# Optimization experiments

Hardware: AMD Instinct MI355X
Metric: run time of the kernel (lower is better)

Reference implementation:

```python
import jax, jax.numpy as jnp
import numpy as np

N = 50000      # nodes
E = 1600000    # edges (before self loops)
B = 512        # graphs
D = 128        # gcn dim (constant across the 3 GAT layers)
H = 1024       # hidden_dim
O = 128        # output_dim
NEG_SLOPE = 0.2


def setup_inputs() -> dict:
    key = jax.random.key(0)
    ks = jax.random.split(key, 24)
    inp = {
        "x": jax.random.normal(ks[0], (N, D), jnp.float32),
        "edge_index": jax.random.randint(ks[1], (2, E), 0, N, dtype=jnp.int64),
        "edge_weight": jax.random.uniform(ks[2], (E,), jnp.float32),
        "batch": jnp.sort(jax.random.randint(ks[3], (N,), 0, B, dtype=jnp.int64)),
    }
    s = 1.0 / np.sqrt(D)
    for i in range(3):
        k = 4 + 4 * i
        inp[f"W{i+1}"] = jax.random.normal(ks[k], (D, D), jnp.float32) * s
        inp[f"as{i+1}"] = jax.random.normal(ks[k + 1], (D,), jnp.float32) * s
        inp[f"ad{i+1}"] = jax.random.normal(ks[k + 2], (D,), jnp.float32) * s
        inp[f"b{i+1}"] = jnp.zeros((D,), jnp.float32)
    inp["Wf1"] = jax.random.normal(ks[16], (D, H), jnp.float32) * s
    inp["bf1"] = jnp.zeros((H,), jnp.float32)
    inp["Wf2"] = jax.random.normal(ks[17], (H, O), jnp.float32) * (1.0 / np.sqrt(H))
    inp["bf2"] = jnp.zeros((O,), jnp.float32)
    return inp


def gat_conv(x, src, dst, W, a_src, a_dst, b):
    """PyG GATConv, heads=1: gather -> leakyrelu -> segment softmax -> scatter-add."""
    h = x @ W                                   # [N, D]
    e = jax.nn.leaky_relu(jnp.take(h @ a_src, src) + jnp.take(h @ a_dst, dst), NEG_SLOPE)  # [E']
    m = jax.ops.segment_max(e, dst, num_segments=N)
    ex = jnp.exp(e - m[dst])
    denom = jax.ops.segment_sum(ex, dst, num_segments=N)
    alpha = ex / denom[dst]                      # segment softmax over incoming edges
    out = jax.ops.segment_sum(alpha[:, None] * h[src], dst, num_segments=N)
    return out + b


def reference(x, edge_index, edge_weight, batch,
              W1, as1, ad1, b1, W2, as2, ad2, b2, W3, as3, ad3, b3,
              Wf1, bf1, Wf2, bf2):
    # GATConv adds self loops; edge_weight is unused by GATConv (faithful to original)
    loop = jnp.arange(N, dtype=edge_index.dtype)
    src = jnp.concatenate([edge_index[0], loop])
    dst = jnp.concatenate([edge_index[1], loop])

    h = gat_conv(x, src, dst, W1, as1, ad1, b1)
    h = jax.nn.relu(gat_conv(h, src, dst, W2, as2, ad2, b2))
    h = jax.nn.relu(gat_conv(h, src, dst, W3, as3, ad3, b3))

    # global mean pool (gep)
    sums = jax.ops.segment_sum(h, batch, num_segments=B)        # [B, D]
    counts = jax.ops.segment_sum(jnp.ones((N,), h.dtype), batch, num_segments=B)
    pooled = sums / jnp.maximum(counts, 1.0)[:, None]

    # MLP head; dropout is identity at inference
    o = jax.nn.relu(pooled) @ Wf1 + bf1
    o = jax.nn.relu(o) @ Wf2 + bf2
    return o
```

## Files before the change

kernel.cpp:

```cpp
#include <hip/hip_runtime.h>
#include <cstdint>
#include <cstddef>

#define NEG_SLOPE 0.2f

__device__ __forceinline__ unsigned enc_f(float f) {
  unsigned u = __float_as_uint(f);
  return (u & 0x80000000u) ? ~u : (u | 0x80000000u);
}
__device__ __forceinline__ float dec_f(unsigned u) {
  return (u & 0x80000000u) ? __uint_as_float(u ^ 0x80000000u) : __uint_as_float(~u);
}
__device__ __forceinline__ unsigned short f2bf(float f) {
  unsigned u = __float_as_uint(f);
  unsigned r = u + 0x7fffu + ((u >> 16) & 1u);
  return (unsigned short)(r >> 16);
}
#define BLO(u) __uint_as_float((u) << 16)
#define BHI(u) __uint_as_float((u) & 0xffff0000u)

__global__ void k_init(int* counts, unsigned* maxPart, int N) {
  int n = blockIdx.x * blockDim.x + threadIdx.x;
  if (n < N) counts[n] = 1;
  if (n < 768) maxPart[n] = 0u;
}

__global__ void k_count_rank(const int* __restrict__ dst, int E,
                             int* counts, int* __restrict__ rank) {
  int e = blockIdx.x * blockDim.x + threadIdx.x;
  if (e < E) rank[e] = atomicAdd(&counts[dst[e]], 1);
}

__global__ __launch_bounds__(1024) void k_scan1(const int* __restrict__ counts, int N,
                                                int* __restrict__ row_ptr, int* __restrict__ part) {
  __shared__ int tmp[1024];
  int t = threadIdx.x;
  int i = blockIdx.x * 1024 + t;
  int v = (i < N) ? counts[i] : 0;
  tmp[t] = v;
  __syncthreads();
  for (int off = 1; off < 1024; off <<= 1) {
    int u = (t >= off) ? tmp[t - off] : 0;
    __syncthreads();
    tmp[t] += u;
    __syncthreads();
  }
  if (i < N) row_ptr[i + 1] = tmp[t];
  if (t == 1023) part[blockIdx.x] = tmp[t];
}

__global__ void k_scan2(int* part, int nb, int* row_ptr) {
  if (threadIdx.x == 0 && blockIdx.x == 0) {
    int run = 0;
    for (int b = 0; b < nb; b++) { int v = part[b]; part[b] = run; run += v; }
    row_ptr[0] = 0;
  }
}

__global__ __launch_bounds__(1024) void k_scan3(int* __restrict__ row_ptr,
                                                const int* __restrict__ part, int N) {
  int i = blockIdx.x * 1024 + threadIdx.x;
  if (i < N) row_ptr[i + 1] += part[blockIdx.x];
}

__global__ void k_fill(const int* __restrict__ src, const int* __restrict__ dst,
                       const int* __restrict__ rank, int E, int N,
                       const int* __restrict__ row_ptr, int* __restrict__ col) {
  int i = blockIdx.x * blockDim.x + threadIdx.x;
  if (i < N) col[row_ptr[i]] = i;
  int e = i - N;
  if (e >= 0 && e < E) col[row_ptr[dst[e]] + rank[e]] = src[e];
}

#define CK 64
__global__ __launch_bounds__(256) void k_gemm_fused(const float* __restrict__ A,
                                                    const float* __restrict__ W,
                                                    unsigned short* __restrict__ hb,
                                                    const float* __restrict__ asrc,
                                                    const float* __restrict__ adst,
                                                    float* __restrict__ sv, float* __restrict__ dv,
                                                    unsigned* __restrict__ maxSlot, int M) {
  __shared__ float As[32][CK + 4];
  __shared__ float Ws[CK][128];
  __shared__ float redmax[4];
  const int K = 128, Nc = 128;
  int t = threadIdx.x;
  int tx = t & 31;
  int ty = t >> 5;
  int rowbase = blockIdx.x * 32;
  float4 acc[4];
  acc[0] = acc[1] = acc[2] = acc[3] = make_float4(0.f, 0.f, 0.f, 0.f);

  for (int kb = 0; kb < K; kb += CK) {
    for (int idx = t * 4; idx < 32 * CK; idx += 256 * 4) {
      int r = idx / CK, kk = idx % CK;
      int gr = rowbase + r;
      float4 v = make_float4(0.f, 0.f, 0.f, 0.f);
      if (gr < M) v = *(const float4*)&A[(size_t)gr * K + kb + kk];
      *(float4*)&As[r][kk] = v;
    }
    for (int idx = t * 4; idx < CK * 128; idx += 256 * 4) {
      int kk = idx >> 7, cc = idx & 127;
      *(float4*)&Ws[kk][cc] = *(const float4*)&W[(size_t)(kb + kk) * Nc + cc];
    }
    __syncthreads();
#pragma unroll
    for (int kk = 0; kk < CK; kk++) {
      float4 w = *(float4*)&Ws[kk][tx * 4];
#pragma unroll
      for (int r = 0; r < 4; r++) {
        float a = As[ty + 8 * r][kk];
        acc[r].x += a * w.x; acc[r].y += a * w.y; acc[r].z += a * w.z; acc[r].w += a * w.w;
      }
    }
    __syncthreads();
  }

  float4 av  = *(const float4*)&asrc[tx * 4];
  float4 adv = *(const float4*)&adst[tx * 4];
  float wmax = -1e30f;
#pragma unroll
  for (int r = 0; r < 4; r++) {
    int gr = rowbase + ty + 8 * r;
    float4 o = acc[r];
    float ps = o.x * av.x + o.y * av.y + o.z * av.z + o.w * av.w;
    float pd = o.x * adv.x + o.y * adv.y + o.z * adv.z + o.w * adv.w;
#pragma unroll
    for (int mask = 16; mask; mask >>= 1) {
      ps += __shfl_xor(ps, mask);
      pd += __shfl_xor(pd, mask);
    }
    if (gr < M) {
      ushort4 hv;
      hv.x = f2bf(o.x); hv.y = f2bf(o.y); hv.z = f2bf(o.z); hv.w = f2bf(o.w);
      *(ushort4*)&hb[(size_t)gr * 128 + tx * 4] = hv;
      if (tx == 0) { sv[gr] = ps; dv[gr] = pd; }
      wmax = fmaxf(wmax, ps);
    }
  }
#pragma unroll
  for (int mask = 32; mask; mask >>= 1) wmax = fmaxf(wmax, __shfl_xor(wmax, mask));
  if ((t & 63) == 0) redmax[t >> 6] = wmax;
  __syncthreads();
  if (t == 0) {
    float mx = fmaxf(fmaxf(redmax[0], redmax[1]), fmaxf(redmax[2], redmax[3]));
    atomicMax(&maxSlot[blockIdx.x & 255], enc_f(mx));
  }
}

__global__ __launch_bounds__(256) void k_agg(const unsigned short* __restrict__ hb,
                                             const float* __restrict__ sv,
                                             const float* __restrict__ dv,
                                             const int* __restrict__ row_ptr,
                                             const int* __restrict__ col,
                                             const float* __restrict__ bias,
                                             const unsigned* __restrict__ maxSlot,
                                             float* __restrict__ out, int N, int relu) {
  int wid = (int)((blockIdx.x * (size_t)blockDim.x + threadIdx.x) >> 6);
  int lane = threadIdx.x & 63;
  if (wid >= N) return;

  unsigned mp = max(max(maxSlot[lane], maxSlot[lane + 64]),
                    max(maxSlot[lane + 128], maxSlot[lane + 192]));
#pragma unroll
  for (int off = 32; off; off >>= 1) mp = max(mp, __shfl_xor(mp, off));
  float maxS = dec_f(mp);

  int beg = row_ptr[wid], end = row_ptr[wid + 1];
  float dn = dv[wid];
  float m = maxS + dn;
  m = (m > 0.f) ? m : NEG_SLOPE * m;

  int g = lane >> 4, sub = lane & 15;
  const uint32_t* hbu = (const uint32_t*)hb;
  float acc[8];
#pragma unroll
  for (int k = 0; k < 8; k++) acc[k] = 0.f;
  float dsum = 0.f;

  for (int j = beg + g; j < end; j += 4) {
    int sn = col[j];
    float e = sv[sn] + dn;
    e = (e > 0.f) ? e : NEG_SLOPE * e;
    float wgt = __expf(e - m);
    dsum += wgt;
    uint4 hv = *(const uint4*)(hbu + (size_t)sn * 64 + sub * 4);
    acc[0] += wgt * BLO(hv.x); acc[1] += wgt * BHI(hv.x);
    acc[2] += wgt * BLO(hv.y); acc[3] += wgt * BHI(hv.y);
    acc[4] += wgt * BLO(hv.z); acc[5] += wgt * BHI(hv.z);
    acc[6] += wgt * BLO(hv.w); acc[7] += wgt * BHI(hv.w);
  }
  dsum += __shfl_xor(dsum, 16);
  dsum += __shfl_xor(dsum, 32);
#pragma unroll
  for (int k = 0; k < 8; k++) {
    acc[k] += __shfl_xor(acc[k], 16);
    acc[k] += __shfl_xor(acc[k], 32);
  }
  if (lane < 16) {
    float inv = 1.f / dsum;
    float4 b0 = *(const float4*)&bias[sub * 8];
    float4 b1 = *(const float4*)&bias[sub * 8 + 4];
    float4 o0, o1;
    o0.x = acc[0] * inv + b0.x; o0.y = acc[1] * inv + b0.y;
    o0.z = acc[2] * inv + b0.z; o0.w = acc[3] * inv + b0.w;
    o1.x = acc[4] * inv + b1.x; o1.y = acc[5] * inv + b1.y;
    o1.z = acc[6] * inv + b1.z; o1.w = acc[7] * inv + b1.w;
    if (relu) {
      o0.x = fmaxf(o0.x, 0.f); o0.y = fmaxf(o0.y, 0.f); o0.z = fmaxf(o0.z, 0.f); o0.w = fmaxf(o0.w, 0.f);
      o1.x = fmaxf(o1.x, 0.f); o1.y = fmaxf(o1.y, 0.f); o1.z = fmaxf(o1.z, 0.f); o1.w = fmaxf(o1.w, 0.f);
    }
    float* op = &out[(size_t)wid * 128 + sub * 8];
    *(float4*)op = o0;
    *(float4*)(op + 4) = o1;
  }
}

__global__ void k_bounds(const int* __restrict__ batch, int N, int B, int* __restrict__ gstart) {
  int n = blockIdx.x * blockDim.x + threadIdx.x;
  if (n >= N) return;
  int cur = batch[n];
  if (n == 0) {
    for (int g = 0; g <= cur; g++) gstart[g] = 0;
  } else {
    int prev = batch[n - 1];
    for (int g = prev + 1; g <= cur; g++) gstart[g] = n;
  }
  if (n == N - 1) {
    for (int g = cur + 1; g <= B; g++) gstart[g] = N;
  }
}

__global__ __launch_bounds__(128) void k_pool(const float* __restrict__ h,
                                              const int* __restrict__ gstart,
                                              float* __restrict__ pooled, int B) {
  int b = blockIdx.x, c = threadIdx.x;
  int s0 = gstart[b], s1 = gstart[b + 1];
  float acc = 0.f;
  for (int n = s0; n < s1; n++) acc += h[(size_t)n * 128 + c];
  int cnt = s1 - s0;
  float p = acc / (float)(cnt > 0 ? cnt : 1);
  pooled[b * 128 + c] = fmaxf(p, 0.f);
}

__global__ __launch_bounds__(256) void k_mlp(const float* __restrict__ pooled,
                                             const float* __restrict__ Wf1,
                                             const float* __restrict__ bf1,
                                             const float* __restrict__ Wf2,
                                             const float* __restrict__ bf2,
                                             float* __restrict__ out, int B) {
  __shared__ float P[4][128];
  __shared__ float H1[4][1024];
  __shared__ float R[4][128];
  int t = threadIdx.x;
  int g0 = blockIdx.x * 4;

  for (int i = t; i < 4 * 128; i += 256) {
    int gi = i >> 7, c = i & 127;
    P[gi][c] = (g0 + gi < B) ? pooled[(size_t)(g0 + gi) * 128 + c] : 0.f;
  }
  __syncthreads();

#pragma unroll
  for (int cb = 0; cb < 4; cb++) {
    int c = cb * 256 + t;
    float a0 = 0.f, a1 = 0.f, a2 = 0.f, a3 = 0.f;
    for (int k = 0; k < 128; k++) {
      float w = Wf1[(size_t)k * 1024 + c];
      a0 += P[0][k] * w; a1 += P[1][k] * w; a2 += P[2][k] * w; a3 += P[3][k] * w;
    }
    float b = bf1[c];
    H1[0][c] = fmaxf(a0 + b, 0.f);
    H1[1][c] = fmaxf(a1 + b, 0.f);
    H1[2][c] = fmaxf(a2 + b, 0.f);
    H1[3][c] = fmaxf(a3 + b, 0.f);
  }
  __syncthreads();

  int c = t & 127, hh = t >> 7;
  float a0 = 0.f, a1 = 0.f, a2 = 0.f, a3 = 0.f;
  int k0 = hh * 512;
  for (int k = k0; k < k0 + 512; k++) {
    float w = Wf2[(size_t)k * 128 + c];
    a0 += H1[0][k] * w; a1 += H1[1][k] * w; a2 += H1[2][k] * w; a3 += H1[3][k] * w;
  }
  if (hh == 1) { R[0][c] = a0; R[1][c] = a1; R[2][c] = a2; R[3][c] = a3; }
  __syncthreads();
  if (hh == 0) {
    float b = bf2[c];
    float o0 = a0 + R[0][c] + b;
    float o1 = a1 + R[1][c] + b;
    float o2 = a2 + R[2][c] + b;
    float o3 = a3 + R[3][c] + b;
    if (g0 + 0 < B) out[(size_t)(g0 + 0) * 128 + c] = o0;
    if (g0 + 1 < B) out[(size_t)(g0 + 1) * 128 + c] = o1;
    if (g0 + 2 < B) out[(size_t)(g0 + 2) * 128 + c] = o2;
    if (g0 + 3 < B) out[(size_t)(g0 + 3) * 128 + c] = o3;
  }
}

extern "C" void kernel_launch(void* const* d_in, const int* in_sizes, int n_in,
                              void* d_out, int out_size, void* d_ws, size_t ws_size,
                              hipStream_t stream) {
  const float* x     = (const float*)d_in[0];
  const int*   ei    = (const int*)d_in[1];
  const int*   batch = (const int*)d_in[3];
  const float* W1 = (const float*)d_in[4];
  const float* as1 = (const float*)d_in[5];
  const float* ad1 = (const float*)d_in[6];
  const float* b1 = (const float*)d_in[7];
  const float* W2 = (const float*)d_in[8];
  const float* as2 = (const float*)d_in[9];
  const float* ad2 = (const float*)d_in[10];
  const float* b2 = (const float*)d_in[11];
  const float* W3 = (const float*)d_in[12];
  const float* as3 = (const float*)d_in[13];
  const float* ad3 = (const float*)d_in[14];
  const float* b3 = (const float*)d_in[15];
  const float* Wf1 = (const float*)d_in[16];
  const float* bf1 = (const float*)d_in[17];
  const float* Wf2 = (const float*)d_in[18];
  const float* bf2 = (const float*)d_in[19];

  const int N = in_sizes[0] / 128;
  const int E = in_sizes[1] / 2;
  const int B = out_size / 128;

  char* base = (char*)d_ws;
  size_t off = 0;
  auto carve = [&](size_t bytes) -> void* {
    off = (off + 255) & ~(size_t)255;
    void* p = base + off;
    off += bytes;
    return p;
  };
  int* counts   = (int*)carve((size_t)N * 4);
  int* row_ptr  = (int*)carve((size_t)(N + 1) * 4);
  int* rank     = (int*)carve((size_t)E * 4);
  int* col      = (int*)carve((size_t)(E + N) * 4);
  int* part     = (int*)carve(1024 * 4);
  int* gstart   = (int*)carve((size_t)(B + 1) * 4);
  unsigned* maxPart = (unsigned*)carve(768 * 4);
  float* sbuf   = (float*)carve((size_t)N * 4);
  float* dbuf   = (float*)carve((size_t)N * 4);
  unsigned short* hb = (unsigned short*)carve((size_t)N * 128 * 2);
  float* abuf   = (float*)carve((size_t)N * 128 * 4);
  float* pooled = (float*)carve((size_t)B * 128 * 4);

  const int* srcp = ei;
  const int* dstp = ei + E;
  const int nb = (N + 1023) / 1024;

  hipLaunchKernelGGL(k_init, dim3((N + 255) / 256), dim3(256), 0, stream, counts, maxPart, N);
  hipLaunchKernelGGL(k_count_rank, dim3((E + 255) / 256), dim3(256), 0, stream, dstp, E, counts, rank);
  hipLaunchKernelGGL(k_scan1, dim3(nb), dim3(1024), 0, stream, counts, N, row_ptr, part);
  hipLaunchKernelGGL(k_scan2, dim3(1), dim3(64), 0, stream, part, nb, row_ptr);
  hipLaunchKernelGGL(k_scan3, dim3(nb), dim3(1024), 0, stream, row_ptr, part, N);
  hipLaunchKernelGGL(k_fill, dim3((E + N + 255) / 256), dim3(256), 0, stream,
                     srcp, dstp, rank, E, N, row_ptr, col);
  hipLaunchKernelGGL(k_bounds, dim3((N + 255) / 256), dim3(256), 0, stream, batch, N, B, gstart);

  const float* Wl[3] = {W1, W2, W3};
  const float* al[3] = {as1, as2, as3};
  const float* dl[3] = {ad1, ad2, ad3};
  const float* bl[3] = {b1, b2, b3};
  const float* cur = x;
  for (int L = 0; L < 3; L++) {
    hipLaunchKernelGGL(k_gemm_fused, dim3((N + 31) / 32), dim3(256), 0, stream,
                       cur, Wl[L], hb, al[L], dl[L], sbuf, dbuf, maxPart + L * 256, N);
    hipLaunchKernelGGL(k_agg, dim3((N + 3) / 4), dim3(256), 0, stream,
                       hb, sbuf, dbuf, row_ptr, col, bl[L], maxPart + L * 256, abuf, N, (L > 0) ? 1 : 0);
    cur = abuf;
  }

  hipLaunchKernelGGL(k_pool, dim3(B), dim3(128), 0, stream, abuf, gstart, pooled, B);
  hipLaunchKernelGGL(k_mlp, dim3((B + 3) / 4), dim3(256), 0, stream,
                     pooled, Wf1, bf1, Wf2, bf2, (float*)d_out, B);
}
```

Baseline: 606.6 us.

## Use f16 MFMA for node GEMM and vectorize CSR build kernels

```diff
diff --git a/kernel.cpp b/kernel.cpp
--- a/kernel.cpp
+++ b/kernel.cpp
@@ -3,6 +3,9 @@
 #include <cstddef>
 
 #define NEG_SLOPE 0.2f
+
+typedef _Float16 f16x8 __attribute__((ext_vector_type(8)));
+typedef float f32x4v __attribute__((ext_vector_type(4)));
 
 __device__ __forceinline__ unsigned enc_f(float f) {
   unsigned u = __float_as_uint(f);
@@ -27,6 +30,21 @@
 
 __global__ void k_count_rank(const int* __restrict__ dst, int E,
                              int* counts, int* __restrict__ rank) {
+  int i = (blockIdx.x * blockDim.x + threadIdx.x) * 4;
+  if (i + 3 < E) {
+    int4 d = *(const int4*)&dst[i];
+    int4 r;
+    r.x = atomicAdd(&counts[d.x], 1);
+    r.y = atomicAdd(&counts[d.y], 1);
+    r.z = atomicAdd(&counts[d.z], 1);
+    r.w = atomicAdd(&counts[d.w], 1);
+    *(int4*)&rank[i] = r;
+  } else {
+    for (int e = i; e < E; e++) rank[e] = atomicAdd(&counts[dst[e]], 1);
+  }
+}
+__global__ void k_count_rank_s(const int* __restrict__ dst, int E,
+                               int* counts, int* __restrict__ rank) {
   int e = blockIdx.x * blockDim.x + threadIdx.x;
   if (e < E) rank[e] = atomicAdd(&counts[dst[e]], 1);
 }
@@ -63,16 +81,37 @@
   if (i < N) row_ptr[i + 1] += part[blockIdx.x];
 }
 
+__global__ void k_fill_self(const int* __restrict__ row_ptr, int* __restrict__ col, int N) {
+  int n = blockIdx.x * blockDim.x + threadIdx.x;
+  if (n < N) col[row_ptr[n]] = n;
+}
+
 __global__ void k_fill(const int* __restrict__ src, const int* __restrict__ dst,
-                       const int* __restrict__ rank, int E, int N,
+                       const int* __restrict__ rank, int E,
                        const int* __restrict__ row_ptr, int* __restrict__ col) {
-  int i = blockIdx.x * blockDim.x + threadIdx.x;
-  if (i < N) col[row_ptr[i]] = i;
-  int e = i - N;
-  if (e >= 0 && e < E) col[row_ptr[dst[e]] + rank[e]] = src[e];
-}
-
-#define CK 64
+  int i = (blockIdx.x * blockDim.x + threadIdx.x) * 4;
+  if (i + 3 < E) {
+    int4 s = *(const int4*)&src[i];
+    int4 d = *(const int4*)&dst[i];
+    int4 r = *(const int4*)&rank[i];
+    col[row_ptr[d.x] + r.x] = s.x;
+    col[row_ptr[d.y] + r.y] = s.y;
+    col[row_ptr[d.z] + r.z] = s.z;
+    col[row_ptr[d.w] + r.w] = s.w;
+  } else {
+    for (int e = i; e < E; e++) col[row_ptr[dst[e]] + rank[e]] = src[e];
+  }
+}
+__global__ void k_fill_s(const int* __restrict__ src, const int* __restrict__ dst,
+                         const int* __restrict__ rank, int E,
+                         const int* __restrict__ row_ptr, int* __restrict__ col) {
+  int e = blockIdx.x * blockDim.x + threadIdx.x;
+  if (e < E) col[row_ptr[dst[e]] + rank[e]] = src[e];
+}
+
+#define AST 136
+#define WST 136
+#define HST 132
 __global__ __launch_bounds__(256) void k_gemm_fused(const float* __restrict__ A,
                                                     const float* __restrict__ W,
                                                     unsigned short* __restrict__ hb,
@@ -80,62 +119,89 @@
                                                     const float* __restrict__ adst,
                                                     float* __restrict__ sv, float* __restrict__ dv,
                                                     unsigned* __restrict__ maxSlot, int M) {
-  __shared__ float As[32][CK + 4];
-  __shared__ float Ws[CK][128];
+  __shared__ __align__(16) char smem[64 * AST * 2 + 128 * WST * 2];
+  _Float16* Ah = (_Float16*)smem;
+  _Float16* Wt = (_Float16*)(smem + 64 * AST * 2);
+  float*    hS = (float*)(smem + 64 * AST * 2);
   __shared__ float redmax[4];
-  const int K = 128, Nc = 128;
   int t = threadIdx.x;
-  int tx = t & 31;
-  int ty = t >> 5;
-  int rowbase = blockIdx.x * 32;
-  float4 acc[4];
-  acc[0] = acc[1] = acc[2] = acc[3] = make_float4(0.f, 0.f, 0.f, 0.f);
-
-  for (int kb = 0; kb < K; kb += CK) {
-    for (int idx = t * 4; idx < 32 * CK; idx += 256 * 4) {
-      int r = idx / CK, kk = idx % CK;
-      int gr = rowbase + r;
-      float4 v = make_float4(0.f, 0.f, 0.f, 0.f);
-      if (gr < M) v = *(const float4*)&A[(size_t)gr * K + kb + kk];
-      *(float4*)&As[r][kk] = v;
+  int rowbase = blockIdx.x * 64;
+
+  for (int i = t; i < 64 * 32; i += 256) {
+    int r = i >> 5, c4 = (i & 31) << 2;
+    int gr = rowbase + r;
+    float4 v = make_float4(0.f, 0.f, 0.f, 0.f);
+    if (gr < M) v = *(const float4*)&A[(size_t)gr * 128 + c4];
+    _Float16 tmp[4] = {(_Float16)v.x, (_Float16)v.y, (_Float16)v.z, (_Float16)v.w};
+    *(short4*)&Ah[r * AST + c4] = *(short4*)tmp;
+  }
+  for (int i = t; i < 128 * 32; i += 256) {
+    int r = i >> 5, c4 = (i & 31) << 2;
+    float4 v = *(const float4*)&W[(size_t)r * 128 + c4];
+    Wt[(c4 + 0) * WST + r] = (_Float16)v.x;
+    Wt[(c4 + 1) * WST + r] = (_Float16)v.y;
+    Wt[(c4 + 2) * WST + r] = (_Float16)v.z;
+    Wt[(c4 + 3) * WST + r] = (_Float16)v.w;
+  }
+  __syncthreads();
+
+  int wave = t >> 6, lane = t & 63, quad = lane >> 4, l15 = lane & 15;
+  f32x4v acc[4][2];
+#pragma unroll
+  for (int mt = 0; mt < 4; mt++)
+#pragma unroll
+    for (int nt = 0; nt < 2; nt++) {
+      acc[mt][nt][0] = 0.f; acc[mt][nt][1] = 0.f; acc[mt][nt][2] = 0.f; acc[mt][nt][3] = 0.f;
     }
-    for (int idx = t * 4; idx < CK * 128; idx += 256 * 4) {
-      int kk = idx >> 7, cc = idx & 127;
-      *(float4*)&Ws[kk][cc] = *(const float4*)&W[(size_t)(kb + kk) * Nc + cc];
-    }
-    __syncthreads();
-#pragma unroll
-    for (int kk = 0; kk < CK; kk++) {
-      float4 w = *(float4*)&Ws[kk][tx * 4];
-#pragma unroll
-      for (int r = 0; r < 4; r++) {
-        float a = As[ty + 8 * r][kk];
-        acc[r].x += a * w.x; acc[r].y += a * w.y; acc[r].z += a * w.z; acc[r].w += a * w.w;
-      }
-    }
-    __syncthreads();
-  }
-
+
+#pragma unroll
+  for (int s = 0; s < 4; s++) {
+    int k0 = (s << 5) + (quad << 3);
+    f16x8 af[4], bf[2];
+#pragma unroll
+    for (int mt = 0; mt < 4; mt++)
+      af[mt] = *(f16x8*)&Ah[(mt * 16 + l15) * AST + k0];
+#pragma unroll
+    for (int nt = 0; nt < 2; nt++)
+      bf[nt] = *(f16x8*)&Wt[(wave * 32 + nt * 16 + l15) * WST + k0];
+#pragma unroll
+    for (int mt = 0; mt < 4; mt++)
+#pragma unroll
+      for (int nt = 0; nt < 2; nt++)
+        acc[mt][nt] = __builtin_amdgcn_mfma_f32_16x16x32_f16(af[mt], bf[nt], acc[mt][nt], 0, 0, 0);
+  }
+  __syncthreads();
+
+#pragma unroll
+  for (int mt = 0; mt < 4; mt++)
+#pragma unroll
+    for (int nt = 0; nt < 2; nt++)
+#pragma unroll
+      for (int rr = 0; rr < 4; rr++)
+        hS[(mt * 16 + quad * 4 + rr) * HST + wave * 32 + nt * 16 + l15] = acc[mt][nt][rr];
+  __syncthreads();
+
+  int tx = t & 31, ty = t >> 5;
   float4 av  = *(const float4*)&asrc[tx * 4];
   float4 adv = *(const float4*)&adst[tx * 4];
   float wmax = -1e30f;
 #pragma unroll
-  for (int r = 0; r < 4; r++) {
-    int gr = rowbase + ty + 8 * r;
-    float4 o = acc[r];
-    float ps = o.x * av.x + o.y * av.y + o.z * av.z + o.w * av.w;
-    float pd = o.x * adv.x + o.y * adv.y + o.z * adv.z + o.w * adv.w;
+  for (int r8 = 0; r8 < 8; r8++) {
+    int row = r8 * 8 + ty;
+    int gr = rowbase + row;
+    float4 hv = *(float4*)&hS[row * HST + tx * 4];
+    float ps = hv.x * av.x + hv.y * av.y + hv.z * av.z + hv.w * av.w;
+    float pd = hv.x * adv.x + hv.y * adv.y + hv.z * adv.z + hv.w * adv.w;
 #pragma unroll
     for (int mask = 16; mask; mask >>= 1) {
       ps += __shfl_xor(ps, mask);
       pd += __shfl_xor(pd, mask);
     }
     if (gr < M) {
-      ushort4 hv;
-      hv.x = f2bf(o.x); hv.y = f2bf(o.y); hv.z = f2bf(o.z); hv.w = f2bf(o.w);
-      *(ushort4*)&hb[(size_t)gr * 128 + tx * 4] = hv;
-      if (tx == 0) { sv[gr] = ps; dv[gr] = pd; }
-      wmax = fmaxf(wmax, ps);
+      ushort4 hq;
+      hq.x = f2bf(hv.x); hq.y = f2bf(hv.y); hq.z = f2bf(hv.z); hq.w = f2bf(hv.w);
+      *(ushort4*)&hb[(size_t)gr * 128 + tx * 4] = hq;
+      if (tx == 0) { sv[gr] = ps; dv[gr] = pd; wmax = fmaxf(wmax, ps); }
     }
   }
 #pragma unroll
@@ -352,12 +418,22 @@
   const int nb = (N + 1023) / 1024;
 
   hipLaunchKernelGGL(k_init, dim3((N + 255) / 256), dim3(256), 0, stream, counts, maxPart, N);
-  hipLaunchKernelGGL(k_count_rank, dim3((E + 255) / 256), dim3(256), 0, stream, dstp, E, counts, rank);
+  if ((E & 3) == 0) {
+    int nq = E / 4;
+    hipLaunchKernelGGL(k_count_rank, dim3((nq + 255) / 256), dim3(256), 0, stream, dstp, E, counts, rank);
+  } else {
+    hipLaunchKernelGGL(k_count_rank_s, dim3((E + 255) / 256), dim3(256), 0, stream, dstp, E, counts, rank);
+  }
   hipLaunchKernelGGL(k_scan1, dim3(nb), dim3(1024), 0, stream, counts, N, row_ptr, part);
   hipLaunchKernelGGL(k_scan2, dim3(1), dim3(64), 0, stream, part, nb, row_ptr);
   hipLaunchKernelGGL(k_scan3, dim3(nb), dim3(1024), 0, stream, row_ptr, part, N);
-  hipLaunchKernelGGL(k_fill, dim3((E + N + 255) / 256), dim3(256), 0, stream,
-                     srcp, dstp, rank, E, N, row_ptr, col);
+  hipLaunchKernelGGL(k_fill_self, dim3((N + 255) / 256), dim3(256), 0, stream, row_ptr, col, N);
+  if ((E & 3) == 0) {
+    int nq = E / 4;
+    hipLaunchKernelGGL(k_fill, dim3((nq + 255) / 256), dim3(256), 0, stream, srcp, dstp, rank, E, row_ptr, col);
+  } else {
+    hipLaunchKernelGGL(k_fill_s, dim3((E + 255) / 256), dim3(256), 0, stream, srcp, dstp, rank, E, row_ptr, col);
+  }
   hipLaunchKernelGGL(k_bounds, dim3((N + 255) / 256), dim3(256), 0, stream, batch, N, B, gstart);
 
   const float* Wl[3] = {W1, W2, W3};
@@ -366,7 +442,7 @@
   const float* bl[3] = {b1, b2, b3};
   const float* cur = x;
   for (int L = 0; L < 3; L++) {
-    hipLaunchKernelGGL(k_gemm_fused, dim3((N + 31) / 32), dim3(256), 0, stream,
+    hipLaunchKernelGGL(k_gemm_fused, dim3((N + 63) / 64), dim3(256), 0, stream,
                        cur, Wl[L], hb, al[L], dl[L], sbuf, dbuf, maxPart + L * 256, N);
     hipLaunchKernelGGL(k_agg, dim3((N + 3) / 4), dim3(256), 0, stream,
                        hb, sbuf, dbuf, row_ptr, col, bl[L], maxPart + L * 256, abuf, N, (L > 0) ? 1 : 0);
```

Measured after the change: 580.6 us. -4.3%, faster.
